# Optimization experiments

Measured on AMD Instinct MI355X. Metric: run time of the kernel, lower is better.

The kernel has to match this reference:

```python
import jax, jax.numpy as jnp
import numpy as np

R_CUTOFF = 5.0
BASIS = 8
NMAX = 8
NSPECIES = 3
EMBED = 16


def _chebyshev_basis(r, r_cutoff, basis_size):
    fc = jnp.where(r < r_cutoff, 0.5 * jnp.cos(jnp.pi * r / r_cutoff) + 0.5, 0.0)
    x = 2.0 * (r / r_cutoff) ** 2 - 1.0
    polys = [jnp.ones_like(x), x]
    for n in range(2, basis_size):
        polys.append(2.0 * x * polys[-1] - polys[-2])
    basis = jnp.stack(polys[:basis_size], axis=-1)  # [E, basis]
    return 0.5 * (basis + 1.0) * fc[:, None]


def setup_inputs() -> dict:
    key = jax.random.key(0)
    ks = jax.random.split(key, 12)
    N, K = 20000, 32
    E = N * K
    positions = jax.random.normal(ks[0], (N, 3), dtype=jnp.float32)
    species = jax.random.randint(ks[1], (N,), 0, NSPECIES, dtype=jnp.int32)
    magmoms = jax.random.normal(ks[2], (N, 3), dtype=jnp.float32)
    # i-major edge list: exactly K edges per atom, grouped by center atom.
    i_idx = jnp.repeat(jnp.arange(N, dtype=jnp.int32), K)
    j_idx = jax.random.randint(ks[3], (E,), 0, N, dtype=jnp.int32)
    edge_index = jnp.stack([i_idx, j_idx], axis=0)
    shifts = jnp.zeros((E, 3), dtype=jnp.float32)
    rb_coefficients = 0.1 * jax.random.normal(ks[4], (NSPECIES * NSPECIES, NMAX, BASIS), dtype=jnp.float32)
    species_embedding = 0.1 * jax.random.normal(ks[5], (NSPECIES, EMBED), dtype=jnp.float32)
    struct_dim = NMAX + NMAX * (NMAX + 1)  # 80
    mag_dim = 3 + 7 * NMAX + 3 * NMAX * NMAX  # 251
    return {
        'positions': positions, 'species': species, 'magmoms': magmoms,
        'edge_index': edge_index, 'shifts': shifts,
        'rb_coefficients': rb_coefficients, 'species_embedding': species_embedding,
        'struct_shift': jnp.zeros(struct_dim, jnp.float32),
        'struct_scale': jnp.ones(struct_dim, jnp.float32),
        'mag_shift': jnp.zeros(mag_dim, jnp.float32),
        'mag_scale': jnp.ones(mag_dim, jnp.float32),
        'atomic_energy_shift': 0.1 * jax.random.normal(ks[6], (NSPECIES,), dtype=jnp.float32),
        'w_struct': 0.05 * jax.random.normal(ks[7], (EMBED + struct_dim,), dtype=jnp.float32),
        'b_struct': 0.05 * jax.random.normal(ks[8], (1,), dtype=jnp.float32),
        'w_mag': 0.05 * jax.random.normal(ks[9], (EMBED + mag_dim,), dtype=jnp.float32),
        'b_mag': 0.05 * jax.random.normal(ks[10], (1,), dtype=jnp.float32),
    }


def _forward(positions, magmoms, shifts, rb_coefficients, species_embedding,
             struct_shift, struct_scale, mag_shift, mag_scale, atomic_energy_shift,
             w_struct, b_struct, w_mag, b_mag, species, edge_index):
    N = positions.shape[0]
    E = edge_index.shape[1]
    K = E // N  # regular neighbor count (edge list is i-major)
    i_idx, j_idx = edge_index[0], edge_index[1]
    r_ij = positions[j_idx] - positions[i_idx] + shifts          # [E,3]
    dist = jnp.linalg.norm(r_ij, axis=-1)                        # [E]
    f_k = _chebyshev_basis(dist, R_CUTOFF, BASIS)                # [E,basis]
    pair_idx = species[i_idx] * NSPECIES + species[j_idx]
    phi = jnp.einsum('enk,ek->en', rb_coefficients[pair_idx], f_k)  # [E,n]
    seg = lambda x: jax.ops.segment_sum(x, i_idx, num_segments=N)
    d = jnp.maximum(dist, 1e-8)[:, None]
    r_hat = r_ij / d
    # --- structural descriptors ---
    d_radial = seg(phi)                                          # [N,n]
    P = seg(phi[:, :, None] * r_hat[:, None, :])                 # [N,n,3]
    PP = jnp.einsum('ina,ima->inm', P, P)
    tu = np.triu_indices(NMAX)
    d_ang_l1 = PP[:, tu[0], tu[1]]
    eye3 = jnp.eye(3, dtype=r_ij.dtype)
    traceless = r_hat[:, :, None] * r_hat[:, None, :] - eye3 / 3.0  # [E,3,3]
    Q = seg(phi[:, :, None, None] * traceless[:, None, :, :])       # [N,n,3,3]
    Qf = Q.reshape(N, NMAX, 9)
    QQ = jnp.einsum('ina,ima->inm', Qf, Qf)
    d_ang_l2 = QQ[:, tu[0], tu[1]]
    desc_struct = jnp.concatenate([d_radial, d_ang_l1, d_ang_l2], axis=-1)
    # --- magnetic descriptors ---
    u = jnp.sum(magmoms * magmoms, axis=-1)                      # [N]
    m_norm = jnp.linalg.norm(magmoms, axis=-1, keepdims=True)
    m_dir = jnp.where(m_norm > 1e-8, magmoms / jnp.maximum(m_norm, 1e-8), 0.0)
    M = seg(phi[:, :, None] * m_dir[j_idx][:, None, :])          # [N,n,3]
    # A_{nm}(i) = sum_{a<b within atom i's edge block} phi_n(a) phi_m(b) (r_a x r_b)
    phi_g = phi.reshape(N, K, NMAX)
    r_g = r_ij.reshape(N, K, 3)
    cross = jnp.cross(r_g[:, :, None, :], r_g[:, None, :, :])    # [N,K,K,3]
    mask = jnp.triu(jnp.ones((K, K), dtype=phi.dtype), k=1)
    tmp = jnp.einsum('iabd,ab,ibm->iamd', cross, mask, phi_g)    # [N,K,3,n]
    A = jnp.einsum('ian,iamd->inmd', phi_g, tmp)                 # [N,n,n,3]
    d_amp = jnp.stack([u, u ** 2, u ** 3], axis=-1)
    d_iso = jnp.sum(m_dir[:, None, :] * M, axis=-1)              # [N,n]
    Qm = jnp.einsum('anij,aj->ani', Q, m_dir)
    d_sia = jnp.sum(m_dir[:, None, :] * Qm, axis=-1)
    mQ = jnp.einsum('ai,amij->amj', m_dir, Q)
    d_sae = jnp.einsum('amj,anj->amn', mQ, M).reshape(N, -1)
    m_cross_M = jnp.cross(jnp.broadcast_to(m_dir[:, None, :], M.shape), M)
    d_dmi = jnp.einsum('inmd,imd->inm', A, m_cross_M).reshape(N, -1)
    u_col = u[:, None]
    d_amp_mix = jnp.concatenate([u_col * d_iso, u_col * d_sia, u_col * d_dmi], axis=-1)
    u_j = u[j_idx]
    d_nbr_amp = seg(phi * u_j[:, None])
    W = seg(phi[:, :, None] * (u_j[:, None] * m_dir[j_idx])[:, None, :])
    d_nbr_amp_ex = jnp.sum(m_dir[:, None, :] * W, axis=-1)
    d_nbr_amp_ex_mix = u_col * d_nbr_amp_ex
    desc_mag = jnp.concatenate([d_amp, d_iso, d_sia, d_sae, d_dmi, d_amp_mix,
                                d_nbr_amp, d_nbr_amp_ex, d_nbr_amp_ex_mix], axis=-1)
    # --- scaling + linear readout heads + per-species shift ---
    ds = (desc_struct - struct_shift) / struct_scale
    dm = (desc_mag - mag_shift) / mag_scale
    emb = species_embedding[species]
    e_struct = jnp.concatenate([emb, ds], axis=-1) @ w_struct + b_struct[0]
    e_mag = jnp.concatenate([emb, dm], axis=-1) @ w_mag + b_mag[0]
    return e_struct + e_mag + atomic_energy_shift[species]        # [N]


def reference(positions, species, magmoms, edge_index, shifts, rb_coefficients,
              species_embedding, struct_shift, struct_scale, mag_shift, mag_scale,
              atomic_energy_shift, w_struct, b_struct, w_mag, b_mag):
    return _forward(positions, magmoms, shifts, rb_coefficients, species_embedding,
                    struct_shift, struct_scale, mag_shift, mag_scale, atomic_energy_shift,
                    w_struct, b_struct, w_mag, b_mag, species, edge_index)
```

## Files before the change

### kernel.cpp

```cpp
#include <hip/hip_runtime.h>

#define NSPEC  3
#define EMBEDD 16
#define KMAX   32
#define RCUT   5.0f
#define PADR   36

typedef float v2f __attribute__((ext_vector_type(2)));

__constant__ int TUN[36] = {0,0,0,0,0,0,0,0, 1,1,1,1,1,1,1, 2,2,2,2,2,2, 3,3,3,3,3, 4,4,4,4, 5,5,5, 6,6, 7};
__constant__ int TUM[36] = {0,1,2,3,4,5,6,7, 1,2,3,4,5,6,7, 2,3,4,5,6,7, 3,4,5,6,7, 4,5,6,7, 5,6,7, 6,7, 7};


template<int CTRL, int RMASK, bool BC>
__device__ __forceinline__ float dpp_mov0(float x) {
    return __int_as_float(__builtin_amdgcn_update_dpp(
        0, __float_as_int(x), CTRL, RMASK, 0xF, BC));
}
__device__ __forceinline__ float prefix32(float x) {
    x += dpp_mov0<0x111, 0xF, true >(x);
    x += dpp_mov0<0x112, 0xF, true >(x);
    x += dpp_mov0<0x114, 0xF, true >(x);
    x += dpp_mov0<0x118, 0xF, true >(x);
    x += dpp_mov0<0x142, 0xA, false>(x);
    return x;
}
__device__ __forceinline__ float swz_xor16(float x) {
    return __int_as_float(__builtin_amdgcn_ds_swizzle(__float_as_int(x), 0x401F));
}
__device__ __forceinline__ float red_k4(float x) {
    x += dpp_mov0<0x128, 0xF, true>(x);
    x += swz_xor16(x);
    return x;
}
__device__ __forceinline__ v2f red_k4_v2(v2f v) {
    v2f t;
    t.x = dpp_mov0<0x128, 0xF, true>(v.x);
    t.y = dpp_mov0<0x128, 0xF, true>(v.y);
    v += t;
    t.x = swz_xor16(v.x);
    t.y = swz_xor16(v.y);
    v += t;
    return v;
}
__device__ __forceinline__ float red32(float x) {
    x += dpp_mov0<0x121, 0xF, true>(x);
    x += dpp_mov0<0x122, 0xF, true>(x);
    x += dpp_mov0<0x124, 0xF, true>(x);
    x += dpp_mov0<0x128, 0xF, true>(x);
    x += swz_xor16(x);
    return x;
}
__device__ __forceinline__ void lds_fence() {
    asm volatile("s_waitcnt lgkmcnt(0)" ::: "memory");
}

struct __align__(16) AtomLds {
    float phiT[8 * PADR];
    float rhx[KMAX], rhy[KMAX], rhz[KMAX];
    float mdx[KMAX], mdy[KMAX], mdz[KMAX];
    float uj[KMAX];
    float P4[8*4];
    float Q8[8*8];
    float M4[8*4];
    float mQ4[8*4];
    float wv4[8*4];
};

__device__ void do_setup(const float* sshift, const float* sscale,
                         const float* mshift, const float* mscale,
                         const float* wstruct, const float* bstruct,
                         const float* wmag, const float* bmag,
                         float* ws)
{
    __shared__ float red[4];
    const int t = threadIdx.x;
    float c = 0.0f;
    for (int idx = t; idx < 80; idx += 256) {
        const float w = wstruct[16 + idx] / sscale[idx];
        ws[idx] = w;
        c += w * sshift[idx];
    }
    for (int idx = t; idx < 251; idx += 256) {
        const float w = wmag[16 + idx] / mscale[idx];
        ws[80 + idx] = w;
        c += w * mshift[idx];
    }
    if (t < EMBEDD) ws[332 + t] = wstruct[t] + wmag[t];
    if (t < 64) {
        ws[400 + t] = wmag[16 + 83 + t]  / mscale[83 + t];
        ws[464 + t] = wmag[16 + 163 + t] / mscale[163 + t];
    }
    #pragma unroll
    for (int d = 1; d <= 32; d <<= 1) c += __shfl_xor(c, d, 64);
    if ((t & 63) == 0) red[t >> 6] = c;
    __syncthreads();
    if (t == 0) ws[331] = bstruct[0] + bmag[0] - (red[0] + red[1] + red[2] + red[3]);
}

__global__ __launch_bounds__(256)
void magpot_prep(const float* __restrict__ pos,
                 const int*   __restrict__ species,
                 const float* __restrict__ mag,
                 const float* __restrict__ sshift, const float* __restrict__ sscale,
                 const float* __restrict__ mshift, const float* __restrict__ mscale,
                 const float* __restrict__ wstruct, const float* __restrict__ bstruct,
                 const float* __restrict__ wmag, const float* __restrict__ bmag,
                 float* __restrict__ ws,
                 int N, int nAtomBlocks)
{
    if ((int)blockIdx.x == nAtomBlocks) {
        do_setup(sshift, sscale, mshift, mscale, wstruct, bstruct, wmag, bmag, ws);
        return;
    }
    const int t = blockIdx.x * 256 + threadIdx.x;
    if (t >= N) return;
    const float px = pos[3*t+0], py = pos[3*t+1], pz = pos[3*t+2];
    const float mx = mag[3*t+0], my = mag[3*t+1], mz = mag[3*t+2];
    const float u = mx*mx + my*my + mz*mz;
    const float minv = (u > 1e-16f) ? __builtin_amdgcn_rsqf(u) : 0.0f;
    float4* atabA = (float4*)(ws + 2048);
    float4* atabB = (float4*)(ws + 2048) + N;
    atabA[t] = make_float4(px, py, pz, __int_as_float(species[t]));
    atabB[t] = make_float4(mx*minv, my*minv, mz*minv, u);
}

__global__ __launch_bounds__(256)
void magpot_main(const int*   __restrict__ eidx,
                 const float* __restrict__ shifts,
                 const float* __restrict__ rb,
                 const float* __restrict__ semb,
                 const float* __restrict__ aes,
                 const float* __restrict__ ws,
                 float* __restrict__ out,
                 int N, int E, int K)
{
    __shared__ AtomLds lds[8];

    const int lane64 = threadIdx.x & 63;
    const int wv     = threadIdx.x >> 6;
    const int h      = lane64 >> 5;
    const int s      = lane64 & 31;
    const int ea     = 31 - s;
    const int i      = blockIdx.x * 8 + wv * 2 + h;
    const bool valid = (i < N);
    const int isafe  = valid ? i : 0;
    AtomLds& L = lds[wv * 2 + h];

    const float* wm = ws + 80;
    const float4* atabA = (const float4*)(ws + 2048);
    const float4* atabB = atabA + N;

    const float4 Ai = atabA[isafe];
    const float4 Bi = atabB[isafe];
    const float pix = Ai.x, piy = Ai.y, piz = Ai.z;
    const int   spi = __float_as_int(Ai.w);
    const float mix = Bi.x, miy = Bi.y, miz = Bi.z;
    const float u_i = Bi.w;

    float phi[8];
    float rx = 0.0f, ry = 0.0f, rz = 0.0f;
    #pragma unroll
    for (int n = 0; n < 8; ++n) phi[n] = 0.0f;

    if (ea < K) {
        const int e = isafe * K + ea;
        const int j = eidx[E + e];
        const float4 Aj = atabA[j];
        const float4 Bj = atabB[j];
        rx = Aj.x - pix + shifts[3*e+0];
        ry = Aj.y - piy + shifts[3*e+1];
        rz = Aj.z - piz + shifts[3*e+2];
        const float d2 = rx*rx + ry*ry + rz*rz;
        const float dist = __builtin_amdgcn_sqrtf(d2);
        const float fc = (dist < RCUT)
            ? (0.5f * __builtin_amdgcn_cosf(dist * 0.1f) + 0.5f)
            : 0.0f;
        const float xr = dist * (1.0f/RCUT);
        const float x  = 2.0f * xr * xr - 1.0f;
        v2f f2[4];
        {
            float fp[8];
            float Tm2 = 1.0f, Tm1 = x;
            fp[0] = 0.5f * (Tm2 + 1.0f) * fc;
            fp[1] = 0.5f * (Tm1 + 1.0f) * fc;
            #pragma unroll
            for (int k = 2; k < 8; ++k) {
                const float T = 2.0f * x * Tm1 - Tm2;
                Tm2 = Tm1; Tm1 = T;
                fp[k] = 0.5f * (T + 1.0f) * fc;
            }
            f2[0] = (v2f){fp[0], fp[1]};
            f2[1] = (v2f){fp[2], fp[3]};
            f2[2] = (v2f){fp[4], fp[5]};
            f2[3] = (v2f){fp[6], fp[7]};
        }
        const int spj = __float_as_int(Aj.w);
        const float4* rb4 = (const float4*)(rb + (spi * NSPEC + spj) * 64);
        #pragma unroll
        for (int n = 0; n < 8; ++n) {
            const float4 r0 = rb4[n*2+0];
            const float4 r1 = rb4[n*2+1];
            v2f a2 = f2[0] * (v2f){r0.x, r0.y};
            a2 += f2[1] * (v2f){r0.z, r0.w};
            a2 += f2[2] * (v2f){r1.x, r1.y};
            a2 += f2[3] * (v2f){r1.z, r1.w};
            const float ph = a2.x + a2.y;
            phi[n] = ph;
            L.phiT[n*PADR + ea] = ph;
        }
        const float dinv = (dist > 1e-8f) ? __builtin_amdgcn_rcpf(dist) : 1e8f;
        L.rhx[ea] = rx * dinv;
        L.rhy[ea] = ry * dinv;
        L.rhz[ea] = rz * dinv;
        L.mdx[ea] = Bj.x;
        L.mdy[ea] = Bj.y;
        L.mdz[ea] = Bj.z;
        L.uj[ea]  = Bj.w;
    } else {
        #pragma unroll
        for (int n = 0; n < 8; ++n) L.phiT[n*PADR + ea] = 0.0f;
        L.rhx[ea] = 0.0f; L.rhy[ea] = 0.0f; L.rhz[ea] = 0.0f;
        L.mdx[ea] = 0.0f; L.mdy[ea] = 0.0f; L.mdz[ea] = 0.0f;
        L.uj[ea] = 0.0f;
    }
    lds_fence();

    float p = 0.0f;

    {
        const int k4 = s >> 3;
        const int n  = s & 7;
        const float4* phR = (const float4*)&L.phiT[n*PADR + k4*8];
        const float4* hxR = (const float4*)&L.rhx[k4*8];
        const float4* hyR = (const float4*)&L.rhy[k4*8];
        const float4* hzR = (const float4*)&L.rhz[k4*8];
        const float4* dxR = (const float4*)&L.mdx[k4*8];
        const float4* dyR = (const float4*)&L.mdy[k4*8];
        const float4* dzR = (const float4*)&L.mdz[k4*8];
        const float4* ujR = (const float4*)&L.uj[k4*8];

        float s_dr = 0.0f, sP2 = 0.0f, s_nb = 0.0f, sM2 = 0.0f, sW0 = 0.0f;
        v2f A1 = {0,0};
        v2f A3 = {0,0};
        v2f A4 = {0,0};
        v2f A5 = {0,0};
        v2f A6 = {0,0};
        v2f A8 = {0,0};

        auto acc = [&](float ph, float hx, float hy, float hz,
                       float dx, float dy, float dz, float uj) {
            const float phu = ph * uj;
            s_dr += ph;
            s_nb += phu;
            sP2 += ph * hz;
            sM2 += ph * dz;
            sW0 += phu * dx;
            A1 += ph * (v2f){hx, hy};
            A3 += ph * ((v2f){hx, hx} * (v2f){hx, hy});
            A4 += ph * ((v2f){hx, hy} * (v2f){hz, hy});
            A5 += ph * ((v2f){hy, hz} * (v2f){hz, hz});
            A6 += ph * (v2f){dx, dy};
            A8 += phu * (v2f){dy, dz};
        };
        #pragma unroll
        for (int q = 0; q < 2; ++q) {
            const float4 ph4 = phR[q], hx4 = hxR[q], hy4 = hyR[q], hz4 = hzR[q];
            const float4 dx4 = dxR[q], dy4 = dyR[q], dz4 = dzR[q], uj4 = ujR[q];
            acc(ph4.x, hx4.x, hy4.x, hz4.x, dx4.x, dy4.x, dz4.x, uj4.x);
            acc(ph4.y, hx4.y, hy4.y, hz4.y, dx4.y, dy4.y, dz4.y, uj4.y);
            acc(ph4.z, hx4.z, hy4.z, hz4.z, dx4.z, dy4.z, dz4.z, uj4.z);
            acc(ph4.w, hx4.w, hy4.w, hz4.w, dx4.w, dy4.w, dz4.w, uj4.w);
        }
        s_dr = red_k4(s_dr); sP2 = red_k4(sP2); s_nb = red_k4(s_nb);
        sM2 = red_k4(sM2);   sW0 = red_k4(sW0);
        A1 = red_k4_v2(A1); A3 = red_k4_v2(A3); A4 = red_k4_v2(A4);
        A5 = red_k4_v2(A5); A6 = red_k4_v2(A6); A8 = red_k4_v2(A8);

        if (k4 == 0) {
            const float dr3 = s_dr * (1.0f/3.0f);
            const float aP0 = A1.x, aP1 = A1.y, aP2 = sP2;
            const float aQ0 = A3.x - dr3, aQ1 = A3.y, aQ2 = A4.x;
            const float aQ3 = A4.y - dr3, aQ4 = A5.x, aQ5 = A5.y - dr3;
            const float aM0 = A6.x, aM1 = A6.y, aM2 = sM2;
            const float aW0 = sW0, aW1 = A8.x, aW2 = A8.y;

            ((float4*)L.P4)[n]     = make_float4(aP0, aP1, aP2, 0.0f);
            ((float4*)L.Q8)[2*n]   = make_float4(aQ0, aQ1, aQ2, aQ3);
            ((float4*)L.Q8)[2*n+1] = make_float4(aQ4, aQ5, 0.0f, 0.0f);
            ((float4*)L.M4)[n]     = make_float4(aM0, aM1, aM2, 0.0f);
            const float mq0 = aQ0*mix + aQ1*miy + aQ2*miz;
            const float mq1 = aQ1*mix + aQ3*miy + aQ4*miz;
            const float mq2 = aQ2*mix + aQ4*miy + aQ5*miz;
            ((float4*)L.mQ4)[n]    = make_float4(mq0, mq1, mq2, 0.0f);
            ((float4*)L.wv4)[n]    = make_float4(miy*aM2 - miz*aM1,
                                                 miz*aM0 - mix*aM2,
                                                 mix*aM1 - miy*aM0, 0.0f);
            const float diso = mix*aM0 + miy*aM1 + miz*aM2;
            const float dsia = mq0*mix + mq1*miy + mq2*miz;
            const float dnex = mix*aW0 + miy*aW1 + miz*aW2;
            p += s_dr * ws[n] + s_nb * wm[227 + n]
               + diso * wm[3 + n]  + dsia * wm[11 + n]  + dnex * wm[235 + n]
               + u_i * (diso * wm[147 + n] + dsia * wm[155 + n] + dnex * wm[243 + n]);
        }
        if (s == 8) {
            const float u2 = u_i * u_i;
            p += u_i * wm[0] + u2 * wm[1] + u2 * u_i * wm[2];
        }
        if (s < EMBEDD)
            p += semb[spi * EMBEDD + s] * ws[332 + s];
    }
    lds_fence();

    {
        const v2f* cw1 = (const v2f*)(ws + 400);
        const v2f* cw2 = (const v2f*)(ws + 464);
        v2f B1[4] = {{0,0},{0,0},{0,0},{0,0}};
        v2f B2[4] = {{0,0},{0,0},{0,0},{0,0}};
        #pragma unroll
        for (int n = 0; n < 8; ++n) {
            #pragma unroll
            for (int jj = 0; jj < 4; ++jj) {
                B1[jj] += phi[n] * cw1[n*4 + jj];
                B2[jj] += phi[n] * cw2[n*4 + jj];
            }
        }
        v2f Bp[4];
        #pragma unroll
        for (int jj = 0; jj < 4; ++jj) Bp[jj] = B1[jj] + u_i * B2[jj];

        float cdmi = 0.0f;
        #pragma unroll
        for (int m = 0; m < 8; ++m) {
            const float4 wvm = ((const float4*)L.wv4)[m];
            const float vx = phi[m] * rx;
            const float vy = phi[m] * ry;
            const float vz = phi[m] * rz;
            const float Sx = prefix32(vx) - vx;
            const float Sy = prefix32(vy) - vy;
            const float Sz = prefix32(vz) - vz;
            const float cx = ry*Sz - rz*Sy;
            const float cy = rz*Sx - rx*Sz;
            const float cz = rx*Sy - ry*Sx;
            const float Bm = (m & 1) ? Bp[m >> 1].y : Bp[m >> 1].x;
            cdmi = fmaf(Bm, cx*wvm.x + cy*wvm.y + cz*wvm.z, cdmi);
        }
        p += cdmi;
    }

    {
        #pragma unroll
        for (int t2 = 0; t2 < 2; ++t2) {
            const int idx = s + t2*32;
            const int m4 = idx >> 3, n4 = idx & 7;
            const float4 mQm = ((const float4*)L.mQ4)[m4];
            const float4 Mn  = ((const float4*)L.M4)[n4];
            p += (mQm.x*Mn.x + mQm.y*Mn.y + mQm.z*Mn.z) * wm[19 + idx];
        }
        #pragma unroll
        for (int t2 = 0; t2 < 2; ++t2) {
            const int idx = s + t2*32;
            if (idx < 36) {
                const int a = TUN[idx], b = TUM[idx];
                const float4 Pa = ((const float4*)L.P4)[a];
                const float4 Pb = ((const float4*)L.P4)[b];
                const float pp = Pa.x*Pb.x + Pa.y*Pb.y + Pa.z*Pb.z;
                const float4 Qa0 = ((const float4*)L.Q8)[2*a], Qa1 = ((const float4*)L.Q8)[2*a+1];
                const float4 Qb0 = ((const float4*)L.Q8)[2*b], Qb1 = ((const float4*)L.Q8)[2*b+1];
                const float qq = Qa0.x*Qb0.x + Qa0.w*Qb0.w + Qa1.y*Qb1.y
                       + 2.0f*(Qa0.y*Qb0.y + Qa0.z*Qb0.z + Qa1.x*Qb1.x);
                p += pp * ws[8 + idx] + qq * ws[44 + idx];
            }
        }
    }

    p = red32(p);
    if (s == 0 && valid)
        out[i] = p + ws[331] + aes[spi];
}

extern "C" void kernel_launch(void* const* d_in, const int* in_sizes, int n_in,
                              void* d_out, int out_size, void* d_ws, size_t ws_size,
                              hipStream_t stream) {
    const float* pos     = (const float*)d_in[0];
    const int*   spc     = (const int*)  d_in[1];
    const float* mg      = (const float*)d_in[2];
    const int*   eidx    = (const int*)  d_in[3];
    const float* shf     = (const float*)d_in[4];
    const float* rb      = (const float*)d_in[5];
    const float* semb    = (const float*)d_in[6];
    const float* sshift  = (const float*)d_in[7];
    const float* sscale  = (const float*)d_in[8];
    const float* mshift  = (const float*)d_in[9];
    const float* mscale  = (const float*)d_in[10];
    const float* aes     = (const float*)d_in[11];
    const float* wstruct = (const float*)d_in[12];
    const float* bstruct = (const float*)d_in[13];
    const float* wmag    = (const float*)d_in[14];
    const float* bmag    = (const float*)d_in[15];
    float* out = (float*)d_out;
    float* ws  = (float*)d_ws;

    const int N = in_sizes[1];
    const int E = in_sizes[3] / 2;
    const int K = E / N;

    const int nAtomBlocks = (N + 255) / 256;
    hipLaunchKernelGGL(magpot_prep, dim3(nAtomBlocks + 1), dim3(256), 0, stream,
                       pos, spc, mg, sshift, sscale, mshift, mscale,
                       wstruct, bstruct, wmag, bmag, ws, N, nAtomBlocks);
    hipLaunchKernelGGL(magpot_main, dim3((N + 7) / 8), dim3(256), 0, stream,
                       eidx, shf, rb, semb, aes, ws, out, N, E, K);
}
```

Before: 119.9 us.

## Process two atoms per half-wave to interleave independent work and raise ILP

Each 32-lane half-wavefront now handles two atoms instead of one. Phase bodies are split into helper functions and run back-to-back for both atoms, so the two atoms' gathers and computations interleave between the LDS fences. The grid is halved and LDS per block doubles. The aim is to hide gather latency and amortize per-atom fences and reductions through instruction-level parallelism, at the cost of more registers and LDS and therefore possibly lower occupancy.

```diff
diff --git a/kernel.cpp b/kernel.cpp
--- a/kernel.cpp
+++ b/kernel.cpp
@@ -67,6 +67,15 @@
     float wv4[8*4];
 };
 
+struct AtomReg {
+    float phi[8];
+    float rx, ry, rz;
+    float mix, miy, miz, u_i;
+    int   spi;
+    int   i;
+    bool  valid;
+};
+
 __device__ void do_setup(const float* sshift, const float* sscale,
                          const float* mshift, const float* mscale,
                          const float* wstruct, const float* bstruct,
@@ -125,52 +134,30 @@
     atabB[t] = make_float4(mx*minv, my*minv, mz*minv, u);
 }
 
-__global__ __launch_bounds__(256)
-void magpot_main(const int*   __restrict__ eidx,
-                 const float* __restrict__ shifts,
-                 const float* __restrict__ rb,
-                 const float* __restrict__ semb,
-                 const float* __restrict__ aes,
-                 const float* __restrict__ ws,
-                 float* __restrict__ out,
-                 int N, int E, int K)
-{
-    __shared__ AtomLds lds[8];
-
-    const int lane64 = threadIdx.x & 63;
-    const int wv     = threadIdx.x >> 6;
-    const int h      = lane64 >> 5;
-    const int s      = lane64 & 31;
-    const int ea     = 31 - s;
-    const int i      = blockIdx.x * 8 + wv * 2 + h;
-    const bool valid = (i < N);
-    const int isafe  = valid ? i : 0;
-    AtomLds& L = lds[wv * 2 + h];
-
-    const float* wm = ws + 80;
-    const float4* atabA = (const float4*)(ws + 2048);
-    const float4* atabB = atabA + N;
-
+__device__ __forceinline__ void phase1(AtomReg& A, AtomLds& L,
+        const int* __restrict__ eidx, const float* __restrict__ shifts,
+        const float* __restrict__ rb,
+        const float4* __restrict__ atabA, const float4* __restrict__ atabB,
+        int E, int K, int ea)
+{
+    const int isafe = A.valid ? A.i : 0;
     const float4 Ai = atabA[isafe];
     const float4 Bi = atabB[isafe];
-    const float pix = Ai.x, piy = Ai.y, piz = Ai.z;
-    const int   spi = __float_as_int(Ai.w);
-    const float mix = Bi.x, miy = Bi.y, miz = Bi.z;
-    const float u_i = Bi.w;
-
-    float phi[8];
-    float rx = 0.0f, ry = 0.0f, rz = 0.0f;
+    A.spi = __float_as_int(Ai.w);
+    A.mix = Bi.x; A.miy = Bi.y; A.miz = Bi.z; A.u_i = Bi.w;
     #pragma unroll
-    for (int n = 0; n < 8; ++n) phi[n] = 0.0f;
+    for (int n = 0; n < 8; ++n) A.phi[n] = 0.0f;
+    A.rx = 0.0f; A.ry = 0.0f; A.rz = 0.0f;
 
     if (ea < K) {
         const int e = isafe * K + ea;
         const int j = eidx[E + e];
         const float4 Aj = atabA[j];
         const float4 Bj = atabB[j];
-        rx = Aj.x - pix + shifts[3*e+0];
-        ry = Aj.y - piy + shifts[3*e+1];
-        rz = Aj.z - piz + shifts[3*e+2];
+        const float rx = Aj.x - Ai.x + shifts[3*e+0];
+        const float ry = Aj.y - Ai.y + shifts[3*e+1];
+        const float rz = Aj.z - Ai.z + shifts[3*e+2];
+        A.rx = rx; A.ry = ry; A.rz = rz;
         const float d2 = rx*rx + ry*ry + rz*rz;
         const float dist = __builtin_amdgcn_sqrtf(d2);
         const float fc = (dist < RCUT)
@@ -196,7 +183,7 @@
             f2[3] = (v2f){fp[6], fp[7]};
         }
         const int spj = __float_as_int(Aj.w);
-        const float4* rb4 = (const float4*)(rb + (spi * NSPEC + spj) * 64);
+        const float4* rb4 = (const float4*)(rb + (A.spi * NSPEC + spj) * 64);
         #pragma unroll
         for (int n = 0; n < 8; ++n) {
             const float4 r0 = rb4[n*2+0];
@@ -206,7 +193,7 @@
             a2 += f2[2] * (v2f){r1.x, r1.y};
             a2 += f2[3] * (v2f){r1.z, r1.w};
             const float ph = a2.x + a2.y;
-            phi[n] = ph;
+            A.phi[n] = ph;
             L.phiT[n*PADR + ea] = ph;
         }
         const float dinv = (dist > 1e-8f) ? __builtin_amdgcn_rcpf(dist) : 1e8f;
@@ -224,94 +211,92 @@
         L.mdx[ea] = 0.0f; L.mdy[ea] = 0.0f; L.mdz[ea] = 0.0f;
         L.uj[ea] = 0.0f;
     }
-    lds_fence();
-
-    float p = 0.0f;
-
-    {
-        const int k4 = s >> 3;
-        const int n  = s & 7;
-        const float4* phR = (const float4*)&L.phiT[n*PADR + k4*8];
-        const float4* hxR = (const float4*)&L.rhx[k4*8];
-        const float4* hyR = (const float4*)&L.rhy[k4*8];
-        const float4* hzR = (const float4*)&L.rhz[k4*8];
-        const float4* dxR = (const float4*)&L.mdx[k4*8];
-        const float4* dyR = (const float4*)&L.mdy[k4*8];
-        const float4* dzR = (const float4*)&L.mdz[k4*8];
-        const float4* ujR = (const float4*)&L.uj[k4*8];
-
-        float s_dr = 0.0f, sP2 = 0.0f, s_nb = 0.0f, sM2 = 0.0f, sW0 = 0.0f;
-        v2f A1 = {0,0};
-        v2f A3 = {0,0};
-        v2f A4 = {0,0};
-        v2f A5 = {0,0};
-        v2f A6 = {0,0};
-        v2f A8 = {0,0};
-
-        auto acc = [&](float ph, float hx, float hy, float hz,
-                       float dx, float dy, float dz, float uj) {
-            const float phu = ph * uj;
-            s_dr += ph;
-            s_nb += phu;
-            sP2 += ph * hz;
-            sM2 += ph * dz;
-            sW0 += phu * dx;
-            A1 += ph * (v2f){hx, hy};
-            A3 += ph * ((v2f){hx, hx} * (v2f){hx, hy});
-            A4 += ph * ((v2f){hx, hy} * (v2f){hz, hy});
-            A5 += ph * ((v2f){hy, hz} * (v2f){hz, hz});
-            A6 += ph * (v2f){dx, dy};
-            A8 += phu * (v2f){dy, dz};
-        };
-        #pragma unroll
-        for (int q = 0; q < 2; ++q) {
-            const float4 ph4 = phR[q], hx4 = hxR[q], hy4 = hyR[q], hz4 = hzR[q];
-            const float4 dx4 = dxR[q], dy4 = dyR[q], dz4 = dzR[q], uj4 = ujR[q];
-            acc(ph4.x, hx4.x, hy4.x, hz4.x, dx4.x, dy4.x, dz4.x, uj4.x);
-            acc(ph4.y, hx4.y, hy4.y, hz4.y, dx4.y, dy4.y, dz4.y, uj4.y);
-            acc(ph4.z, hx4.z, hy4.z, hz4.z, dx4.z, dy4.z, dz4.z, uj4.z);
-            acc(ph4.w, hx4.w, hy4.w, hz4.w, dx4.w, dy4.w, dz4.w, uj4.w);
-        }
-        s_dr = red_k4(s_dr); sP2 = red_k4(sP2); s_nb = red_k4(s_nb);
-        sM2 = red_k4(sM2);   sW0 = red_k4(sW0);
-        A1 = red_k4_v2(A1); A3 = red_k4_v2(A3); A4 = red_k4_v2(A4);
-        A5 = red_k4_v2(A5); A6 = red_k4_v2(A6); A8 = red_k4_v2(A8);
-
-        if (k4 == 0) {
-            const float dr3 = s_dr * (1.0f/3.0f);
-            const float aP0 = A1.x, aP1 = A1.y, aP2 = sP2;
-            const float aQ0 = A3.x - dr3, aQ1 = A3.y, aQ2 = A4.x;
-            const float aQ3 = A4.y - dr3, aQ4 = A5.x, aQ5 = A5.y - dr3;
-            const float aM0 = A6.x, aM1 = A6.y, aM2 = sM2;
-            const float aW0 = sW0, aW1 = A8.x, aW2 = A8.y;
-
-            ((float4*)L.P4)[n]     = make_float4(aP0, aP1, aP2, 0.0f);
-            ((float4*)L.Q8)[2*n]   = make_float4(aQ0, aQ1, aQ2, aQ3);
-            ((float4*)L.Q8)[2*n+1] = make_float4(aQ4, aQ5, 0.0f, 0.0f);
-            ((float4*)L.M4)[n]     = make_float4(aM0, aM1, aM2, 0.0f);
-            const float mq0 = aQ0*mix + aQ1*miy + aQ2*miz;
-            const float mq1 = aQ1*mix + aQ3*miy + aQ4*miz;
-            const float mq2 = aQ2*mix + aQ4*miy + aQ5*miz;
-            ((float4*)L.mQ4)[n]    = make_float4(mq0, mq1, mq2, 0.0f);
-            ((float4*)L.wv4)[n]    = make_float4(miy*aM2 - miz*aM1,
-                                                 miz*aM0 - mix*aM2,
-                                                 mix*aM1 - miy*aM0, 0.0f);
-            const float diso = mix*aM0 + miy*aM1 + miz*aM2;
-            const float dsia = mq0*mix + mq1*miy + mq2*miz;
-            const float dnex = mix*aW0 + miy*aW1 + miz*aW2;
-            p += s_dr * ws[n] + s_nb * wm[227 + n]
-               + diso * wm[3 + n]  + dsia * wm[11 + n]  + dnex * wm[235 + n]
-               + u_i * (diso * wm[147 + n] + dsia * wm[155 + n] + dnex * wm[243 + n]);
-        }
-        if (s == 8) {
-            const float u2 = u_i * u_i;
-            p += u_i * wm[0] + u2 * wm[1] + u2 * u_i * wm[2];
-        }
-        if (s < EMBEDD)
-            p += semb[spi * EMBEDD + s] * ws[332 + s];
-    }
-    lds_fence();
-
+}
+
+__device__ __forceinline__ void phase2(const AtomReg& A, AtomLds& L, float& p,
+        const float* __restrict__ ws, const float* __restrict__ wm,
+        const float* __restrict__ semb, int s)
+{
+    const int k4 = s >> 3;
+    const int n  = s & 7;
+    const float4* phR = (const float4*)&L.phiT[n*PADR + k4*8];
+    const float4* hxR = (const float4*)&L.rhx[k4*8];
+    const float4* hyR = (const float4*)&L.rhy[k4*8];
+    const float4* hzR = (const float4*)&L.rhz[k4*8];
+    const float4* dxR = (const float4*)&L.mdx[k4*8];
+    const float4* dyR = (const float4*)&L.mdy[k4*8];
+    const float4* dzR = (const float4*)&L.mdz[k4*8];
+    const float4* ujR = (const float4*)&L.uj[k4*8];
+
+    float s_dr = 0.0f, sP2 = 0.0f, s_nb = 0.0f, sM2 = 0.0f, sW0 = 0.0f;
+    v2f A1 = {0,0}, A3 = {0,0}, A4 = {0,0}, A5 = {0,0}, A6 = {0,0}, A8 = {0,0};
+
+    auto acc = [&](float ph, float hx, float hy, float hz,
+                   float dx, float dy, float dz, float uj) {
+        const float phu = ph * uj;
+        s_dr += ph;
+        s_nb += phu;
+        sP2 += ph * hz;
+        sM2 += ph * dz;
+        sW0 += phu * dx;
+        A1 += ph * (v2f){hx, hy};
+        A3 += ph * ((v2f){hx, hx} * (v2f){hx, hy});
+        A4 += ph * ((v2f){hx, hy} * (v2f){hz, hy});
+        A5 += ph * ((v2f){hy, hz} * (v2f){hz, hz});
+        A6 += ph * (v2f){dx, dy};
+        A8 += phu * (v2f){dy, dz};
+    };
+    #pragma unroll
+    for (int q = 0; q < 2; ++q) {
+        const float4 ph4 = phR[q], hx4 = hxR[q], hy4 = hyR[q], hz4 = hzR[q];
+        const float4 dx4 = dxR[q], dy4 = dyR[q], dz4 = dzR[q], uj4 = ujR[q];
+        acc(ph4.x, hx4.x, hy4.x, hz4.x, dx4.x, dy4.x, dz4.x, uj4.x);
+        acc(ph4.y, hx4.y, hy4.y, hz4.y, dx4.y, dy4.y, dz4.y, uj4.y);
+        acc(ph4.z, hx4.z, hy4.z, hz4.z, dx4.z, dy4.z, dz4.z, uj4.z);
+        acc(ph4.w, hx4.w, hy4.w, hz4.w, dx4.w, dy4.w, dz4.w, uj4.w);
+    }
+    s_dr = red_k4(s_dr); sP2 = red_k4(sP2); s_nb = red_k4(s_nb);
+    sM2 = red_k4(sM2);   sW0 = red_k4(sW0);
+    A1 = red_k4_v2(A1); A3 = red_k4_v2(A3); A4 = red_k4_v2(A4);
+    A5 = red_k4_v2(A5); A6 = red_k4_v2(A6); A8 = red_k4_v2(A8);
+
+    if (k4 == 0) {
+        const float dr3 = s_dr * (1.0f/3.0f);
+        const float aP0 = A1.x, aP1 = A1.y, aP2 = sP2;
+        const float aQ0 = A3.x - dr3, aQ1 = A3.y, aQ2 = A4.x;
+        const float aQ3 = A4.y - dr3, aQ4 = A5.x, aQ5 = A5.y - dr3;
+        const float aM0 = A6.x, aM1 = A6.y, aM2 = sM2;
+        const float aW0 = sW0, aW1 = A8.x, aW2 = A8.y;
+
+        ((float4*)L.P4)[n]     = make_float4(aP0, aP1, aP2, 0.0f);
+        ((float4*)L.Q8)[2*n]   = make_float4(aQ0, aQ1, aQ2, aQ3);
+        ((float4*)L.Q8)[2*n+1] = make_float4(aQ4, aQ5, 0.0f, 0.0f);
+        ((float4*)L.M4)[n]     = make_float4(aM0, aM1, aM2, 0.0f);
+        const float mq0 = aQ0*A.mix + aQ1*A.miy + aQ2*A.miz;
+        const float mq1 = aQ1*A.mix + aQ3*A.miy + aQ4*A.miz;
+        const float mq2 = aQ2*A.mix + aQ4*A.miy + aQ5*A.miz;
+        ((float4*)L.mQ4)[n]    = make_float4(mq0, mq1, mq2, 0.0f);
+        ((float4*)L.wv4)[n]    = make_float4(A.miy*aM2 - A.miz*aM1,
+                                             A.miz*aM0 - A.mix*aM2,
+                                             A.mix*aM1 - A.miy*aM0, 0.0f);
+        const float diso = A.mix*aM0 + A.miy*aM1 + A.miz*aM2;
+        const float dsia = mq0*A.mix + mq1*A.miy + mq2*A.miz;
+        const float dnex = A.mix*aW0 + A.miy*aW1 + A.miz*aW2;
+        p += s_dr * ws[n] + s_nb * wm[227 + n]
+           + diso * wm[3 + n]  + dsia * wm[11 + n]  + dnex * wm[235 + n]
+           + A.u_i * (diso * wm[147 + n] + dsia * wm[155 + n] + dnex * wm[243 + n]);
+    }
+    if (s == 8) {
+        const float u2 = A.u_i * A.u_i;
+        p += A.u_i * wm[0] + u2 * wm[1] + u2 * A.u_i * wm[2];
+    }
+    if (s < EMBEDD)
+        p += semb[A.spi * EMBEDD + s] * ws[332 + s];
+}
+
+__device__ __forceinline__ void phase34(const AtomReg& A, AtomLds& L, float& p,
+        const float* __restrict__ ws, const float* __restrict__ wm, int s)
+{
     {
         const v2f* cw1 = (const v2f*)(ws + 400);
         const v2f* cw2 = (const v2f*)(ws + 464);
@@ -321,33 +306,32 @@
         for (int n = 0; n < 8; ++n) {
             #pragma unroll
             for (int jj = 0; jj < 4; ++jj) {
-                B1[jj] += phi[n] * cw1[n*4 + jj];
-                B2[jj] += phi[n] * cw2[n*4 + jj];
+                B1[jj] += A.phi[n] * cw1[n*4 + jj];
+                B2[jj] += A.phi[n] * cw2[n*4 + jj];
             }
         }
         v2f Bp[4];
         #pragma unroll
-        for (int jj = 0; jj < 4; ++jj) Bp[jj] = B1[jj] + u_i * B2[jj];
+        for (int jj = 0; jj < 4; ++jj) Bp[jj] = B1[jj] + A.u_i * B2[jj];
 
         float cdmi = 0.0f;
         #pragma unroll
         for (int m = 0; m < 8; ++m) {
             const float4 wvm = ((const float4*)L.wv4)[m];
-            const float vx = phi[m] * rx;
-            const float vy = phi[m] * ry;
-            const float vz = phi[m] * rz;
+            const float vx = A.phi[m] * A.rx;
+            const float vy = A.phi[m] * A.ry;
+            const float vz = A.phi[m] * A.rz;
             const float Sx = prefix32(vx) - vx;
             const float Sy = prefix32(vy) - vy;
             const float Sz = prefix32(vz) - vz;
-            const float cx = ry*Sz - rz*Sy;
-            const float cy = rz*Sx - rx*Sz;
-            const float cz = rx*Sy - ry*Sx;
+            const float cx = A.ry*Sz - A.rz*Sy;
+            const float cy = A.rz*Sx - A.rx*Sz;
+            const float cz = A.rx*Sy - A.ry*Sx;
             const float Bm = (m & 1) ? Bp[m >> 1].y : Bp[m >> 1].x;
             cdmi = fmaf(Bm, cx*wvm.x + cy*wvm.y + cz*wvm.z, cdmi);
         }
         p += cdmi;
     }
-
     {
         #pragma unroll
         for (int t2 = 0; t2 < 2; ++t2) {
@@ -373,10 +357,54 @@
             }
         }
     }
-
-    p = red32(p);
-    if (s == 0 && valid)
-        out[i] = p + ws[331] + aes[spi];
+}
+
+__global__ __launch_bounds__(256)
+void magpot_main(const int*   __restrict__ eidx,
+                 const float* __restrict__ shifts,
+                 const float* __restrict__ rb,
+                 const float* __restrict__ semb,
+                 const float* __restrict__ aes,
+                 const float* __restrict__ ws,
+                 float* __restrict__ out,
+                 int N, int E, int K)
+{
+    __shared__ AtomLds lds[16];
+
+    const int lane64 = threadIdx.x & 63;
+    const int wv     = threadIdx.x >> 6;
+    const int h      = lane64 >> 5;
+    const int s      = lane64 & 31;
+    const int ea     = 31 - s;
+
+    const float* wm = ws + 80;
+    const float4* atabA = (const float4*)(ws + 2048);
+    const float4* atabB = atabA + N;
+
+    AtomReg R0, R1;
+    R0.i = blockIdx.x * 16 + wv * 2 + h;  R0.valid = (R0.i < N);
+    R1.i = R0.i + 8;                      R1.valid = (R1.i < N);
+    AtomLds& L0 = lds[wv*2 + h];
+    AtomLds& L1 = lds[8 + wv*2 + h];
+
+    phase1(R0, L0, eidx, shifts, rb, atabA, atabB, E, K, ea);
+    phase1(R1, L1, eidx, shifts, rb, atabA, atabB, E, K, ea);
+    lds_fence();
+
+    float p0 = 0.0f, p1 = 0.0f;
+    phase2(R0, L0, p0, ws, wm, semb, s);
+    phase2(R1, L1, p1, ws, wm, semb, s);
+    lds_fence();
+
+    phase34(R0, L0, p0, ws, wm, s);
+    phase34(R1, L1, p1, ws, wm, s);
+
+    p0 = red32(p0);
+    p1 = red32(p1);
+    if (s == 0) {
+        if (R0.valid) out[R0.i] = p0 + ws[331] + aes[R0.spi];
+        if (R1.valid) out[R1.i] = p1 + ws[331] + aes[R1.spi];
+    }
 }
 
 extern "C" void kernel_launch(void* const* d_in, const int* in_sizes, int n_in,
@@ -409,6 +437,6 @@
     hipLaunchKernelGGL(magpot_prep, dim3(nAtomBlocks + 1), dim3(256), 0, stream,
                        pos, spc, mg, sshift, sscale, mshift, mscale,
                        wstruct, bstruct, wmag, bmag, ws, N, nAtomBlocks);
-    hipLaunchKernelGGL(magpot_main, dim3((N + 7) / 8), dim3(256), 0, stream,
+    hipLaunchKernelGGL(magpot_main, dim3((N + 15) / 16), dim3(256), 0, stream,
                        eidx, shf, rb, semb, aes, ws, out, N, E, K);
 }
```

New measurement: 150.0 us. 1.25x slower.
